# Optimization experiments

Hardware: AMD Instinct MI355X
Metric: run time of the kernel (lower is better)

Reference implementation:

```python
import jax, jax.numpy as jnp
import numpy as np

B, T, E, H, V = 64, 21, 512, 512, 10000


def _lstm_step(x, h, c, W_ih, W_hh, b):
    # PyTorch LSTMCell gate order: i, f, g, o
    gates = x @ W_ih.T + h @ W_hh.T + b  # [B, 4H]
    i, f, g, o = jnp.split(gates, 4, axis=-1)
    i, f, o = jax.nn.sigmoid(i), jax.nn.sigmoid(f), jax.nn.sigmoid(o)
    g = jnp.tanh(g)
    c_new = f * c + i * g
    h_new = o * jnp.tanh(c_new)
    return h_new, c_new


def setup_inputs() -> dict:
    key = jax.random.key(0)
    ks = jax.random.split(key, 8)
    s_ih = 1.0 / np.sqrt(H)
    return {
        "features": jax.random.normal(ks[0], (B, E), jnp.float32),
        "caption_embedding": jax.random.normal(ks[1], (B, T, E), jnp.float32),
        "W_ih": jax.random.uniform(ks[2], (4 * H, E), jnp.float32, -s_ih, s_ih),
        "W_hh": jax.random.uniform(ks[3], (4 * H, H), jnp.float32, -s_ih, s_ih),
        "b_ih": jax.random.uniform(ks[4], (4 * H,), jnp.float32, -s_ih, s_ih),
        "b_hh": jax.random.uniform(ks[5], (4 * H,), jnp.float32, -s_ih, s_ih),
        "W_lin": jax.random.uniform(ks[6], (V, H), jnp.float32, -s_ih, s_ih),
        "b_lin": jax.random.uniform(ks[7], (V,), jnp.float32, -s_ih, s_ih),
    }


def reference(features, caption_embedding, W_ih, W_hh, b_ih, b_hh, W_lin, b_lin):
    b = b_ih + b_hh
    batch = features.shape[0]
    hidden = W_hh.shape[1]
    h0 = jnp.zeros((batch, hidden), features.dtype)
    c0 = jnp.zeros((batch, hidden), features.dtype)
    # t = 0: consume image features, no output emitted
    h, c = _lstm_step(features, h0, c0, W_ih, W_hh, b)
    # t = 1..T-1: consume caption_embedding[:, t-1], emit linear(h)
    emb_seq = jnp.swapaxes(caption_embedding[:, :-1, :], 0, 1)  # [T-1, B, E]

    def body(carry, x_t):
        h, c = carry
        h, c = _lstm_step(x_t, h, c, W_ih, W_hh, b)
        out = h @ W_lin.T + b_lin  # [B, V]
        return (h, c), out

    _, outs = jax.lax.scan(body, (h, c), emb_seq)  # [T-1, B, V]
    return jnp.swapaxes(outs, 0, 1)  # [B, T-1, V]
```

## Files before the change

### kernel.cpp

```cpp
#include <hip/hip_runtime.h>
#include <hip/hip_bf16.h>


#define NB 64
#define NT 21
#define NE 512
#define NH 512
#define NV 10000
#define G4 2048
#define FLGD 16

typedef __attribute__((ext_vector_type(8))) short bf16x8;
typedef __attribute__((ext_vector_type(4))) float f32x4;
typedef __attribute__((ext_vector_type(4))) unsigned short u16x4;

#define OFF_WIH_HI   0UL
#define OFF_WIH_LO   2097152UL
#define OFF_WHH_HI   4194304UL
#define OFF_WHH_LO   6291456UL
#define OFF_WLIN_HI  8388608UL
#define OFF_XSEQ_HI  18743296UL
#define OFF_XSEQ_LO  20185088UL
#define OFF_BIAS     21626880UL
#define OFF_XIH      21635072UL
#define OFF_GHH      32645120UL
#define OFF_GHL      32776192UL
#define OFF_C        32907264UL
#define OFF_HBUF     33038336UL
#define OFF_FLG      34349056UL

__device__ inline unsigned short f2bf(float f) {
    unsigned int u = __float_as_uint(f);
    unsigned int r = u + 0x7FFFu + ((u >> 16) & 1u);
    return (unsigned short)(r >> 16);
}
__device__ inline float bf2f(unsigned short s) {
    return __uint_as_float(((unsigned int)s) << 16);
}

__device__ __forceinline__ void gl_lds16(const unsigned short* g, unsigned short* l) {
    auto gp = (const __attribute__((address_space(1))) unsigned int*)(unsigned long long)(const void*)g;
    auto lp = (__attribute__((address_space(3))) unsigned int*)(unsigned int)(unsigned long long)(void*)l;
    __builtin_amdgcn_global_load_lds(gp, lp, 16, 0, 0);
}

__device__ __forceinline__ void gl_lds16_sc(const unsigned short* g, unsigned short* l) {
    auto gp = (const __attribute__((address_space(1))) unsigned int*)(unsigned long long)(const void*)g;
    auto lp = (__attribute__((address_space(3))) unsigned int*)(unsigned int)(unsigned long long)(void*)l;
    __builtin_amdgcn_global_load_lds(gp, lp, 16, 0, 17);
}

__device__ __forceinline__ void st4_sc(unsigned int* p, unsigned int v) {
    asm volatile("global_store_dword %0, %1, off sc0 sc1" :: "v"(p), "v"(v) : "memory");
}
__device__ __forceinline__ void st8_sc(unsigned short* p, u16x4 v) {
    asm volatile("global_store_dwordx2 %0, %1, off sc0 sc1" :: "v"(p), "v"(v) : "memory");
}
__device__ __forceinline__ void st16_sc(float* p, f32x4 v) {
    asm volatile("global_store_dwordx4 %0, %1, off sc0 sc1" :: "v"(p), "v"(v) : "memory");
}

__global__ __launch_bounds__(512) void fused_all(
    const float* __restrict__ features, const float* __restrict__ cap,
    const float* __restrict__ W_ih_f, const float* __restrict__ W_hh_f,
    const float* __restrict__ b_ih, const float* __restrict__ b_hh,
    const float* __restrict__ W_lin_f, const float* __restrict__ b_lin,
    float* __restrict__ out, unsigned char* __restrict__ ws)
{
    __shared__ unsigned short Hhi[64 * 512];
    __shared__ unsigned short Hlo[64 * 512];
    __shared__ float glf[4096];
    const int tid = threadIdx.x;
    const int lane = tid & 63, wv = tid >> 6;
    const int mf = lane & 15, kg = lane >> 4;

    unsigned int* __restrict__ flg = (unsigned int*)(ws + OFF_C);
    unsigned int* __restrict__ slabctr = (unsigned int*)(ws + OFF_FLG);
    unsigned short* __restrict__ hbuf = (unsigned short*)(ws + OFF_HBUF);
    const float* __restrict__ bias = (const float*)(ws + OFF_BIAS);
    float* __restrict__ xih_base = (float*)(ws + OFF_XIH);

    {
        unsigned short* wih_hi = (unsigned short*)(ws + OFF_WIH_HI);
        unsigned short* wih_lo = (unsigned short*)(ws + OFF_WIH_LO);
        unsigned short* xs_hi = (unsigned short*)(ws + OFF_XSEQ_HI);
        unsigned short* xs_lo = (unsigned short*)(ws + OFF_XSEQ_LO);
        float* bias_w = (float*)(ws + OFF_BIAS);
        int idx = blockIdx.x * 512 + tid;
        for (int it = 0; it < 4; ++it, idx += 131072) {
            if (idx < 262144) {
                const int i4 = idx * 4;
                float4 w = *(const float4*)(W_ih_f + i4);
                u16x4 hi, lo;
                hi.x = f2bf(w.x); lo.x = f2bf(w.x - bf2f(hi.x));
                hi.y = f2bf(w.y); lo.y = f2bf(w.y - bf2f(hi.y));
                hi.z = f2bf(w.z); lo.z = f2bf(w.z - bf2f(hi.z));
                hi.w = f2bf(w.w); lo.w = f2bf(w.w - bf2f(hi.w));
                st8_sc(wih_hi + i4, hi);
                st8_sc(wih_lo + i4, lo);
            } else if (idx < 434176) {
                const int i4 = (idx - 262144) * 4;
                const int e = i4 & 511;
                const int b = (i4 >> 9) & 63;
                const int t2 = i4 >> 15;
                float4 x = (t2 == 0) ? *(const float4*)(features + b * NE + e)
                                     : *(const float4*)(cap + b * (NT * NE) + (t2 - 1) * NE + e);
                u16x4 hi, lo;
                hi.x = f2bf(x.x); lo.x = f2bf(x.x - bf2f(hi.x));
                hi.y = f2bf(x.y); lo.y = f2bf(x.y - bf2f(hi.y));
                hi.z = f2bf(x.z); lo.z = f2bf(x.z - bf2f(hi.z));
                hi.w = f2bf(x.w); lo.w = f2bf(x.w - bf2f(hi.w));
                st8_sc(xs_hi + i4, hi);
                st8_sc(xs_lo + i4, lo);
            } else if (idx < 434688) {
                const int j = (idx - 434176) * 4;
                float4 a = *(const float4*)(b_ih + j);
                float4 b = *(const float4*)(b_hh + j);
                f32x4 s;
                s[0] = a.x + b.x; s[1] = a.y + b.y; s[2] = a.z + b.z; s[3] = a.w + b.w;
                st16_sc(bias_w + j, s);
            }
        }
        asm volatile("s_waitcnt vmcnt(0)" ::: "memory");
        __syncthreads();
        if (tid == 0)
            __hip_atomic_fetch_add(&slabctr[24 * FLGD], 1u, __ATOMIC_RELAXED, __HIP_MEMORY_SCOPE_AGENT);
    }

    if (blockIdx.x < 32) {
        const int bc = blockIdx.x;
        const int q = wv & 3;
        const int mh = wv >> 2;

        unsigned short* __restrict__ ghh = (unsigned short*)(ws + OFF_GHH);
        unsigned short* __restrict__ ghl = (unsigned short*)(ws + OFF_GHL);

        bf16x8 bh[16], blo[16];
#pragma unroll
        for (int j = 0; j < 16; ++j) {
            const float* src = W_hh_f + (size_t)(q * 512 + bc * 16 + mf) * 512 + j * 32 + kg * 8;
            float4 w0 = *(const float4*)src;
            float4 w1 = *(const float4*)(src + 4);
            float ff[8] = {w0.x, w0.y, w0.z, w0.w, w1.x, w1.y, w1.z, w1.w};
#pragma unroll
            for (int e = 0; e < 8; ++e) {
                const unsigned short h = f2bf(ff[e]);
                bh[j][e] = (short)h;
                blo[j][e] = (short)f2bf(ff[e] - bf2f(h));
            }
        }

        const int crow = tid >> 3;
        const int cp = tid & 7;
        const int c0 = bc * 16 + cp * 2;
        const int jc0 = c0 >> 3;
        float creg0 = 0.f, creg1 = 0.f;

        float2 xp[4];
        auto load_xp = [&](int tt) {
            const float* __restrict__ xq = xih_base + (size_t)tt * NB * G4;
#pragma unroll
            for (int g2 = 0; g2 < 4; ++g2)
                xp[g2] = *(const float2*)&xq[crow * G4 + g2 * 512 + c0];
        };

        if (tid == 0) {
            while (__hip_atomic_load(&slabctr[0], __ATOMIC_RELAXED, __HIP_MEMORY_SCOPE_AGENT) < 16u)
                __builtin_amdgcn_s_sleep(1);
        }
        __syncthreads();
        load_xp(0);

        for (int t = 0; t < NT; ++t) {
            f32x4 acc[2];
            acc[0] = (f32x4){0.f, 0.f, 0.f, 0.f};
            acc[1] = (f32x4){0.f, 0.f, 0.f, 0.f};

            if (t > 0) {
                const int rd = (t + 1) & 1;
                const unsigned short* __restrict__ ghh_r = ghh + rd * (NB * NH);
                const unsigned short* __restrict__ ghl_r = ghl + rd * (NB * NH);
#pragma unroll
                for (int i = 0; i < 8; ++i) {
                    const int s = i * 512 + tid;
                    gl_lds16_sc(ghh_r + s * 8, &Hhi[s * 8]);
                }
#pragma unroll
                for (int i = 0; i < 8; ++i) {
                    const int s = i * 512 + tid;
                    gl_lds16_sc(ghl_r + s * 8, &Hlo[s * 8]);
                }
                asm volatile("s_waitcnt vmcnt(8)" ::: "memory");
                __builtin_amdgcn_s_barrier();
#pragma unroll
                for (int kt = 0; kt < 16; ++kt) {
                    const int j = kt * 4 + kg;
#pragma unroll
                    for (int m = 0; m < 2; ++m) {
                        const int row = mh * 32 + m * 16 + mf;
                        bf16x8 a_hi = *(const bf16x8*)&Hhi[(row * 64 + (j ^ (row & 7))) * 8];
                        acc[m] = __builtin_amdgcn_mfma_f32_16x16x32_bf16(a_hi, bh[kt], acc[m], 0, 0, 0);
                        acc[m] = __builtin_amdgcn_mfma_f32_16x16x32_bf16(a_hi, blo[kt], acc[m], 0, 0, 0);
                    }
                }
                asm volatile("s_waitcnt vmcnt(0)" ::: "memory");
                __builtin_amdgcn_s_barrier();
#pragma unroll
                for (int kt = 0; kt < 16; ++kt) {
                    const int j = kt * 4 + kg;
#pragma unroll
                    for (int m = 0; m < 2; ++m) {
                        const int row = mh * 32 + m * 16 + mf;
                        bf16x8 a_lo = *(const bf16x8*)&Hlo[(row * 64 + (j ^ (row & 7))) * 8];
                        acc[m] = __builtin_amdgcn_mfma_f32_16x16x32_bf16(a_lo, bh[kt], acc[m], 0, 0, 0);
                    }
                }
            }

#pragma unroll
            for (int m = 0; m < 2; ++m) {
                const int row = mh * 32 + m * 16 + kg * 4;
#pragma unroll
                for (int r = 0; r < 4; ++r)
                    glf[(q * 64 + row + r) * 16 + mf] = acc[m][r];
            }
            __syncthreads();

            {
                unsigned short* __restrict__ ghh_w = ghh + (t & 1) * (NB * NH);
                unsigned short* __restrict__ ghl_w = ghl + (t & 1) * (NB * NH);
                const float2 g0 = *(const float2*)&glf[(0 * 64 + crow) * 16 + cp * 2];
                const float2 g1 = *(const float2*)&glf[(1 * 64 + crow) * 16 + cp * 2];
                const float2 g2 = *(const float2*)&glf[(2 * 64 + crow) * 16 + cp * 2];
                const float2 g3 = *(const float2*)&glf[(3 * 64 + crow) * 16 + cp * 2];
                const float gi0 = g0.x + xp[0].x, gi1 = g0.y + xp[0].y;
                const float gf0 = g1.x + xp[1].x, gf1 = g1.y + xp[1].y;
                const float gg0 = g2.x + xp[2].x, gg1 = g2.y + xp[2].y;
                const float go0 = g3.x + xp[3].x, go1 = g3.y + xp[3].y;
                const float i0 = 1.f / (1.f + __expf(-gi0)), i1 = 1.f / (1.f + __expf(-gi1));
                const float f0 = 1.f / (1.f + __expf(-gf0)), f1 = 1.f / (1.f + __expf(-gf1));
                const float ga0 = tanhf(gg0),                ga1 = tanhf(gg1);
                const float o0 = 1.f / (1.f + __expf(-go0)), o1 = 1.f / (1.f + __expf(-go1));
                const float cn0 = f0 * creg0 + i0 * ga0;
                const float cn1 = f1 * creg1 + i1 * ga1;
                creg0 = cn0; creg1 = cn1;
                const float h0 = o0 * tanhf(cn0);
                const float h1 = o1 * tanhf(cn1);
                const unsigned short hi0 = f2bf(h0), hi1 = f2bf(h1);
                const unsigned short lo0 = f2bf(h0 - bf2f(hi0)), lo1 = f2bf(h1 - bf2f(hi1));
                const unsigned int hpack = (unsigned int)hi0 | ((unsigned int)hi1 << 16);
                const unsigned int lpack = (unsigned int)lo0 | ((unsigned int)lo1 << 16);
                const int sw = crow * 512 + ((jc0 ^ (crow & 7)) << 3) + (cp & 3) * 2;
                st4_sc((unsigned int*)&ghh_w[sw], hpack);
                st4_sc((unsigned int*)&ghl_w[sw], lpack);
                if (t >= 1)
                    st4_sc((unsigned int*)&hbuf[(size_t)(t - 1) * (NB * NH) + crow * NH + c0], hpack);
            }

            asm volatile("s_waitcnt vmcnt(0)" ::: "memory");
            __syncthreads();
            if (tid == 0) {
                unsigned int one = 1u;
                unsigned int* fp = flg + ((size_t)t * 32 + bc) * FLGD;
                asm volatile("global_store_dword %0, %1, off sc0 sc1" :: "v"(fp), "v"(one) : "memory");
            }
            if (t < NT - 1) {
                if (wv == 0) {
                    if (lane < 32) {
                        const unsigned int* fp = flg + ((size_t)t * 32 + lane) * FLGD;
                        while (__hip_atomic_load(fp, __ATOMIC_RELAXED, __HIP_MEMORY_SCOPE_AGENT) == 0u)
                            __builtin_amdgcn_s_sleep(1);
                    } else if (lane == 32) {
                        const unsigned int* sp = slabctr + (size_t)(t + 1) * FLGD;
                        while (__hip_atomic_load(sp, __ATOMIC_RELAXED, __HIP_MEMORY_SCOPE_AGENT) < 16u)
                            __builtin_amdgcn_s_sleep(1);
                    }
                }
                __syncthreads();
                load_xp(t + 1);
            }
        }
        asm volatile("s_waitcnt vmcnt(0)" ::: "memory");
        return;
    }

    const int g = blockIdx.x - 32;
    const int mw2 = (wv >> 2) * 32, nw2 = (wv & 3) * 32;

    if (tid == 0) {
        while (__hip_atomic_load(&slabctr[24 * FLGD], __ATOMIC_RELAXED, __HIP_MEMORY_SCOPE_AGENT) < 256u)
            __builtin_amdgcn_s_sleep(1);
    }
    __syncthreads();

    {
        const unsigned short* __restrict__ xh = (const unsigned short*)(ws + OFF_XSEQ_HI);
        const unsigned short* __restrict__ xl = (const unsigned short*)(ws + OFF_XSEQ_LO);
        const unsigned short* __restrict__ wih_h = (const unsigned short*)(ws + OFF_WIH_HI);
        const unsigned short* __restrict__ wih_l = (const unsigned short*)(ws + OFF_WIH_LO);

        unsigned short* Ah2 = Hhi;
        unsigned short* Al2 = Hhi + 4096;
        unsigned short* Bh2 = Hhi + 8192;
        unsigned short* Bl2 = Hhi + 16384;

        const int ntile = (g < 112) ? 2 : 1;
        for (int p = 0; p < ntile; ++p) {
            const int T = (p == 0) ? g : 224 + g;
            const int slab = T >> 4, ct = T & 15;
            const unsigned short* __restrict__ xhA = xh + (size_t)slab * 64 * 512;
            const unsigned short* __restrict__ xlA = xl + (size_t)slab * 64 * 512;

            auto stageA = [&](int buf, int k0) {
                if (tid < 256) {
                    const int s = tid, r = s >> 2, kc = (s & 3) * 8;
                    gl_lds16(xhA + (size_t)r * 512 + k0 + kc, &Ah2[buf * 2048 + s * 8]);
                    gl_lds16(xlA + (size_t)r * 512 + k0 + kc, &Al2[buf * 2048 + s * 8]);
                } else {
#pragma unroll
                    for (int h2 = 0; h2 < 2; ++h2) {
                        const int s = h2 * 256 + (tid - 256), r = s >> 2, kc = (s & 3) * 8;
                        gl_lds16(wih_h + (size_t)(ct * 128 + r) * 512 + k0 + kc, &Bh2[buf * 4096 + s * 8]);
                        gl_lds16(wih_l + (size_t)(ct * 128 + r) * 512 + k0 + kc, &Bl2[buf * 4096 + s * 8]);
                    }
                }
            };

            f32x4 acc2[2][2];
#pragma unroll
            for (int i = 0; i < 2; i++)
#pragma unroll
                for (int j = 0; j < 2; j++) acc2[i][j] = (f32x4){0.f, 0.f, 0.f, 0.f};

            stageA(0, 0);
            for (int kt = 0; kt < 16; ++kt) {
                __syncthreads();
                const int cur = kt & 1;
                if (kt < 15) stageA(cur ^ 1, (kt + 1) * 32);
                bf16x8 ah_[2], al_[2], bh_[2], bl_[2];
#pragma unroll
                for (int i = 0; i < 2; i++) {
                    ah_[i] = *(const bf16x8*)&Ah2[cur * 2048 + (mw2 + i * 16 + mf) * 32 + kg * 8];
                    al_[i] = *(const bf16x8*)&Al2[cur * 2048 + (mw2 + i * 16 + mf) * 32 + kg * 8];
                    bh_[i] = *(const bf16x8*)&Bh2[cur * 4096 + (nw2 + i * 16 + mf) * 32 + kg * 8];
                    bl_[i] = *(const bf16x8*)&Bl2[cur * 4096 + (nw2 + i * 16 + mf) * 32 + kg * 8];
                }
#pragma unroll
                for (int i = 0; i < 2; i++)
#pragma unroll
                    for (int j = 0; j < 2; j++) {
                        acc2[i][j] = __builtin_amdgcn_mfma_f32_16x16x32_bf16(ah_[i], bh_[j], acc2[i][j], 0, 0, 0);
                        acc2[i][j] = __builtin_amdgcn_mfma_f32_16x16x32_bf16(ah_[i], bl_[j], acc2[i][j], 0, 0, 0);
                        acc2[i][j] = __builtin_amdgcn_mfma_f32_16x16x32_bf16(al_[i], bh_[j], acc2[i][j], 0, 0, 0);
                    }
            }
#pragma unroll
            for (int i = 0; i < 2; i++)
#pragma unroll
                for (int j = 0; j < 2; j++) {
                    const int col = ct * 128 + nw2 + j * 16 + mf;
                    const float bb = bias[col];
#pragma unroll
                    for (int r = 0; r < 4; r++) {
                        const int row = slab * 64 + mw2 + i * 16 + kg * 4 + r;
                        st4_sc((unsigned int*)&xih_base[(size_t)row * G4 + col],
                               __float_as_uint(acc2[i][j][r] + bb));
                    }
                }
            asm volatile("s_waitcnt vmcnt(0)" ::: "memory");
            __syncthreads();
            if (tid == 0)
                __hip_atomic_fetch_add(&slabctr[slab * FLGD], 1u, __ATOMIC_RELAXED, __HIP_MEMORY_SCOPE_AGENT);
            __syncthreads();
        }
    }

    {
        unsigned short* wlin_w = (unsigned short*)(ws + OFF_WLIN_HI);
        int idx = g * 512 + tid;
        for (int it = 0; it < 12; ++it, idx += 114688) {
            if (idx < 1280000) {
                const int i4 = idx * 4;
                float4 w = *(const float4*)(W_lin_f + i4);
                u16x4 hi;
                hi.x = f2bf(w.x); hi.y = f2bf(w.y); hi.z = f2bf(w.z); hi.w = f2bf(w.w);
                st8_sc(wlin_w + i4, hi);
            }
        }
        asm volatile("s_waitcnt vmcnt(0)" ::: "memory");
        __syncthreads();
        if (tid == 0) {
            __hip_atomic_fetch_add(&slabctr[25 * FLGD], 1u, __ATOMIC_RELAXED, __HIP_MEMORY_SCOPE_AGENT);
            while (__hip_atomic_load(&slabctr[25 * FLGD], __ATOMIC_RELAXED, __HIP_MEMORY_SCOPE_AGENT) < 224u)
                __builtin_amdgcn_s_sleep(1);
        }
        __syncthreads();
    }

    const unsigned short* __restrict__ wlin = (const unsigned short*)(ws + OFF_WLIN_HI);
    const int jt = g % 79;
    const int rshare = g / 79;
    const int nshare = (jt < 66) ? 3 : 2;
    const int n0g = jt * 128;

    unsigned short* __restrict__ AsB = Hhi;
    unsigned short* __restrict__ BsB = Hhi + 4096;

    for (int tt = rshare; tt < NT - 1; tt += nshare) {
        if (wv == 0) {
            const unsigned int* fp = flg + ((size_t)(tt + 1) * 32 + (lane & 31)) * FLGD;
            while (__hip_atomic_load(fp, __ATOMIC_RELAXED, __HIP_MEMORY_SCOPE_AGENT) == 0u)
                __builtin_amdgcn_s_sleep(2);
        }
        __syncthreads();

        const unsigned short* __restrict__ hbA = hbuf + (size_t)tt * (NB * NH);
        auto stageC = [&](int buf, int k0) {
            if (tid < 256) {
                const int s = tid;
                const int r = s >> 2, kcol = (s & 3) * 8;
                gl_lds16_sc(hbA + (size_t)r * 512 + k0 + kcol, &AsB[buf * 2048 + s * 8]);
            } else {
#pragma unroll
                for (int h2 = 0; h2 < 2; ++h2) {
                    const int s = h2 * 256 + (tid - 256);
                    const int r = s >> 2, kcol = (s & 3) * 8;
                    gl_lds16(wlin + (size_t)(n0g + r) * 512 + k0 + kcol, &BsB[buf * 4096 + s * 8]);
                }
            }
        };

        f32x4 acc2[2][2];
#pragma unroll
        for (int i = 0; i < 2; i++)
#pragma unroll
            for (int j = 0; j < 2; j++) acc2[i][j] = (f32x4){0.f, 0.f, 0.f, 0.f};

        stageC(0, 0);
        for (int kt = 0; kt < 16; ++kt) {
            __syncthreads();
            const int cur = kt & 1;
            if (kt < 15) stageC(cur ^ 1, (kt + 1) * 32);
            bf16x8 af[2], bfv[2];
#pragma unroll
            for (int i = 0; i < 2; i++) {
                af[i]  = *(const bf16x8*)&AsB[cur * 2048 + (mw2 + i * 16 + mf) * 32 + kg * 8];
                bfv[i] = *(const bf16x8*)&BsB[cur * 4096 + (nw2 + i * 16 + mf) * 32 + kg * 8];
            }
#pragma unroll
            for (int i = 0; i < 2; i++)
#pragma unroll
                for (int j = 0; j < 2; j++)
                    acc2[i][j] = __builtin_amdgcn_mfma_f32_16x16x32_bf16(af[i], bfv[j], acc2[i][j], 0, 0, 0);
        }
#pragma unroll
        for (int i = 0; i < 2; i++)
#pragma unroll
            for (int j = 0; j < 2; j++) {
                const int col = n0g + nw2 + j * 16 + mf;
                if (col < NV) {
                    const float bl = b_lin[col];
#pragma unroll
                    for (int r = 0; r < 4; r++) {
                        const int b_ = mw2 + i * 16 + kg * 4 + r;
                        out[(size_t)b_ * ((NT - 1) * NV) + (size_t)tt * NV + col] = acc2[i][j][r] + bl;
                    }
                }
            }
        __syncthreads();
    }
}

extern "C" void kernel_launch(void* const* d_in, const int* in_sizes, int n_in,
                              void* d_out, int out_size, void* d_ws, size_t ws_size,
                              hipStream_t stream)
{
    const float* features = (const float*)d_in[0];
    const float* cap      = (const float*)d_in[1];
    const float* W_ih     = (const float*)d_in[2];
    const float* W_hh     = (const float*)d_in[3];
    const float* b_ih     = (const float*)d_in[4];
    const float* b_hh     = (const float*)d_in[5];
    const float* W_lin    = (const float*)d_in[6];
    const float* b_lin    = (const float*)d_in[7];
    float* out = (float*)d_out;
    unsigned char* ws = (unsigned char*)d_ws;

    (void)hipMemsetAsync(ws + OFF_C, 0, (size_t)NT * 32 * FLGD * sizeof(unsigned int), stream);
    (void)hipMemsetAsync(ws + OFF_FLG, 0, (size_t)32 * FLGD * sizeof(unsigned int), stream);

    hipLaunchKernelGGL(fused_all, dim3(256), dim3(512), 0, stream,
                       features, cap, W_ih, W_hh, b_ih, b_hh, W_lin, b_lin, out, ws);
}
```

Measured before the change: 269.1 us.

## Move recurrent blocks off weight-conversion prologue and split per-wave flag waits

The 32 recurrent LSTM blocks now skip the shared bf16 hi/lo conversion prologue and start immediately. Only the 224 GEMM blocks do the conversion, with a rebuilt stride and a barrier count of 224. Inside the recurrence, each wave now waits only on the 4 producer flags whose h chunks it loads, then copies those chunks to LDS itself. The h layout changes from a row-major swizzle to a chunk-major layout so each wave's slice is contiguous. This is meant to cut the prologue delay on the serial critical path and the single-wave all-flags barrier per step. The cost is a different LDS read pattern that may bring bank conflicts, and a moved x-projection load.

```diff
diff --git a/kernel.cpp b/kernel.cpp
--- a/kernel.cpp
+++ b/kernel.cpp
@@ -80,14 +80,172 @@
     const float* __restrict__ bias = (const float*)(ws + OFF_BIAS);
     float* __restrict__ xih_base = (float*)(ws + OFF_XIH);
 
+    if (blockIdx.x < 32) {
+        const int bc = blockIdx.x;
+        const int q = wv & 3;
+        const int mh = wv >> 2;
+
+        unsigned short* __restrict__ ghh = (unsigned short*)(ws + OFF_GHH);
+        unsigned short* __restrict__ ghl = (unsigned short*)(ws + OFF_GHL);
+
+        bf16x8 bh[16], blo[16];
+#pragma unroll
+        for (int j = 0; j < 16; ++j) {
+            const float* src = W_hh_f + (size_t)(q * 512 + bc * 16 + mf) * 512 + j * 32 + kg * 8;
+            float4 w0 = *(const float4*)src;
+            float4 w1 = *(const float4*)(src + 4);
+            float ff[8] = {w0.x, w0.y, w0.z, w0.w, w1.x, w1.y, w1.z, w1.w};
+#pragma unroll
+            for (int e = 0; e < 8; ++e) {
+                const unsigned short h = f2bf(ff[e]);
+                bh[j][e] = (short)h;
+                blo[j][e] = (short)f2bf(ff[e] - bf2f(h));
+            }
+        }
+
+        const int crow = tid >> 3;
+        const int cp = tid & 7;
+        const int c0 = bc * 16 + cp * 2;
+        const int jch = bc * 2 + (cp >> 2);
+        const int sw = (jch * 64 + crow) * 8 + ((cp * 2) & 7);
+        float creg0 = 0.f, creg1 = 0.f;
+
+        float2 xp[4];
+        auto load_xp = [&](int tt) {
+            const float* __restrict__ xq = xih_base + (size_t)tt * NB * G4;
+#pragma unroll
+            for (int g2 = 0; g2 < 4; ++g2)
+                xp[g2] = *(const float2*)&xq[crow * G4 + g2 * 512 + c0];
+        };
+
+        if (tid == 0) {
+            while (__hip_atomic_load(&slabctr[0], __ATOMIC_RELAXED, __HIP_MEMORY_SCOPE_AGENT) < 16u)
+                __builtin_amdgcn_s_sleep(1);
+        }
+        __syncthreads();
+        load_xp(0);
+
+        for (int t = 0; t < NT; ++t) {
+            f32x4 acc[2];
+            acc[0] = (f32x4){0.f, 0.f, 0.f, 0.f};
+            acc[1] = (f32x4){0.f, 0.f, 0.f, 0.f};
+
+            if (t > 0) {
+                const int rd = (t + 1) & 1;
+                const unsigned short* __restrict__ ghh_r = ghh + rd * (NB * NH);
+                const unsigned short* __restrict__ ghl_r = ghl + rd * (NB * NH);
+
+                if (lane < 4) {
+                    const unsigned int* fp = flg + ((size_t)(t - 1) * 32 + wv * 4 + lane) * FLGD;
+                    while (__hip_atomic_load(fp, __ATOMIC_RELAXED, __HIP_MEMORY_SCOPE_AGENT) == 0u)
+                        __builtin_amdgcn_s_sleep(1);
+                } else if (lane == 4) {
+                    const unsigned int* sp = slabctr + (size_t)t * FLGD;
+                    while (__hip_atomic_load(sp, __ATOMIC_RELAXED, __HIP_MEMORY_SCOPE_AGENT) < 16u)
+                        __builtin_amdgcn_s_sleep(1);
+                }
+#pragma unroll
+                for (int pp = 0; pp < 4; ++pp) {
+                    const int jj = (wv * 4 + pp) * 2;
+                    gl_lds16_sc(ghh_r + (jj    ) * 512 + lane * 8, &Hhi[(jj    ) * 512 + lane * 8]);
+                    gl_lds16_sc(ghh_r + (jj + 1) * 512 + lane * 8, &Hhi[(jj + 1) * 512 + lane * 8]);
+                }
+#pragma unroll
+                for (int pp = 0; pp < 4; ++pp) {
+                    const int jj = (wv * 4 + pp) * 2;
+                    gl_lds16_sc(ghl_r + (jj    ) * 512 + lane * 8, &Hlo[(jj    ) * 512 + lane * 8]);
+                    gl_lds16_sc(ghl_r + (jj + 1) * 512 + lane * 8, &Hlo[(jj + 1) * 512 + lane * 8]);
+                }
+                asm volatile("s_waitcnt vmcnt(8)" ::: "memory");
+                __builtin_amdgcn_s_barrier();
+                load_xp(t);
+#pragma unroll
+                for (int kt = 0; kt < 16; ++kt) {
+                    const int j = kt * 4 + kg;
+#pragma unroll
+                    for (int m = 0; m < 2; ++m) {
+                        const int row = mh * 32 + m * 16 + mf;
+                        bf16x8 a_hi = *(const bf16x8*)&Hhi[(j * 64 + row) * 8];
+                        acc[m] = __builtin_amdgcn_mfma_f32_16x16x32_bf16(a_hi, bh[kt], acc[m], 0, 0, 0);
+                        acc[m] = __builtin_amdgcn_mfma_f32_16x16x32_bf16(a_hi, blo[kt], acc[m], 0, 0, 0);
+                    }
+                }
+                asm volatile("s_waitcnt vmcnt(0)" ::: "memory");
+                __builtin_amdgcn_s_barrier();
+#pragma unroll
+                for (int kt = 0; kt < 16; ++kt) {
+                    const int j = kt * 4 + kg;
+#pragma unroll
+                    for (int m = 0; m < 2; ++m) {
+                        const int row = mh * 32 + m * 16 + mf;
+                        bf16x8 a_lo = *(const bf16x8*)&Hlo[(j * 64 + row) * 8];
+                        acc[m] = __builtin_amdgcn_mfma_f32_16x16x32_bf16(a_lo, bh[kt], acc[m], 0, 0, 0);
+                    }
+                }
+            }
+
+#pragma unroll
+            for (int m = 0; m < 2; ++m) {
+                const int row = mh * 32 + m * 16 + kg * 4;
+#pragma unroll
+                for (int r = 0; r < 4; ++r)
+                    glf[(q * 64 + row + r) * 16 + mf] = acc[m][r];
+            }
+            __syncthreads();
+
+            {
+                unsigned short* __restrict__ ghh_w = ghh + (t & 1) * (NB * NH);
+                unsigned short* __restrict__ ghl_w = ghl + (t & 1) * (NB * NH);
+                const float2 g0 = *(const float2*)&glf[(0 * 64 + crow) * 16 + cp * 2];
+                const float2 g1 = *(const float2*)&glf[(1 * 64 + crow) * 16 + cp * 2];
+                const float2 g2 = *(const float2*)&glf[(2 * 64 + crow) * 16 + cp * 2];
+                const float2 g3 = *(const float2*)&glf[(3 * 64 + crow) * 16 + cp * 2];
+                const float gi0 = g0.x + xp[0].x, gi1 = g0.y + xp[0].y;
+                const float gf0 = g1.x + xp[1].x, gf1 = g1.y + xp[1].y;
+                const float gg0 = g2.x + xp[2].x, gg1 = g2.y + xp[2].y;
+                const float go0 = g3.x + xp[3].x, go1 = g3.y + xp[3].y;
+                const float i0 = 1.f / (1.f + __expf(-gi0)), i1 = 1.f / (1.f + __expf(-gi1));
+                const float f0 = 1.f / (1.f + __expf(-gf0)), f1 = 1.f / (1.f + __expf(-gf1));
+                const float ga0 = tanhf(gg0),                ga1 = tanhf(gg1);
+                const float o0 = 1.f / (1.f + __expf(-go0)), o1 = 1.f / (1.f + __expf(-go1));
+                const float cn0 = f0 * creg0 + i0 * ga0;
+                const float cn1 = f1 * creg1 + i1 * ga1;
+                creg0 = cn0; creg1 = cn1;
+                const float h0 = o0 * tanhf(cn0);
+                const float h1 = o1 * tanhf(cn1);
+                const unsigned short hi0 = f2bf(h0), hi1 = f2bf(h1);
+                const unsigned short lo0 = f2bf(h0 - bf2f(hi0)), lo1 = f2bf(h1 - bf2f(hi1));
+                const unsigned int hpack = (unsigned int)hi0 | ((unsigned int)hi1 << 16);
+                const unsigned int lpack = (unsigned int)lo0 | ((unsigned int)lo1 << 16);
+                st4_sc((unsigned int*)&ghh_w[sw], hpack);
+                st4_sc((unsigned int*)&ghl_w[sw], lpack);
+                if (t >= 1)
+                    st4_sc((unsigned int*)&hbuf[(size_t)(t - 1) * (NB * NH) + crow * NH + c0], hpack);
+            }
+
+            asm volatile("s_waitcnt vmcnt(0)" ::: "memory");
+            __syncthreads();
+            if (tid == 0) {
+                unsigned int one = 1u;
+                unsigned int* fp = flg + ((size_t)t * 32 + bc) * FLGD;
+                asm volatile("global_store_dword %0, %1, off sc0 sc1" :: "v"(fp), "v"(one) : "memory");
+            }
+        }
+        asm volatile("s_waitcnt vmcnt(0)" ::: "memory");
+        return;
+    }
+
+    const int g = blockIdx.x - 32;
+    const int mw2 = (wv >> 2) * 32, nw2 = (wv & 3) * 32;
+
     {
         unsigned short* wih_hi = (unsigned short*)(ws + OFF_WIH_HI);
         unsigned short* wih_lo = (unsigned short*)(ws + OFF_WIH_LO);
         unsigned short* xs_hi = (unsigned short*)(ws + OFF_XSEQ_HI);
         unsigned short* xs_lo = (unsigned short*)(ws + OFF_XSEQ_LO);
         float* bias_w = (float*)(ws + OFF_BIAS);
-        int idx = blockIdx.x * 512 + tid;
-        for (int it = 0; it < 4; ++it, idx += 131072) {
+        int idx = g * 512 + tid;
+        for (int it = 0; it < 4; ++it, idx += 114688) {
             if (idx < 262144) {
                 const int i4 = idx * 4;
                 float4 w = *(const float4*)(W_ih_f + i4);
@@ -123,175 +281,13 @@
         }
         asm volatile("s_waitcnt vmcnt(0)" ::: "memory");
         __syncthreads();
-        if (tid == 0)
+        if (tid == 0) {
             __hip_atomic_fetch_add(&slabctr[24 * FLGD], 1u, __ATOMIC_RELAXED, __HIP_MEMORY_SCOPE_AGENT);
+            while (__hip_atomic_load(&slabctr[24 * FLGD], __ATOMIC_RELAXED, __HIP_MEMORY_SCOPE_AGENT) < 224u)
+                __builtin_amdgcn_s_sleep(1);
+        }
+        __syncthreads();
     }
-
-    if (blockIdx.x < 32) {
-        const int bc = blockIdx.x;
-        const int q = wv & 3;
-        const int mh = wv >> 2;
-
-        unsigned short* __restrict__ ghh = (unsigned short*)(ws + OFF_GHH);
-        unsigned short* __restrict__ ghl = (unsigned short*)(ws + OFF_GHL);
-
-        bf16x8 bh[16], blo[16];
-#pragma unroll
-        for (int j = 0; j < 16; ++j) {
-            const float* src = W_hh_f + (size_t)(q * 512 + bc * 16 + mf) * 512 + j * 32 + kg * 8;
-            float4 w0 = *(const float4*)src;
-            float4 w1 = *(const float4*)(src + 4);
-            float ff[8] = {w0.x, w0.y, w0.z, w0.w, w1.x, w1.y, w1.z, w1.w};
-#pragma unroll
-            for (int e = 0; e < 8; ++e) {
-                const unsigned short h = f2bf(ff[e]);
-                bh[j][e] = (short)h;
-                blo[j][e] = (short)f2bf(ff[e] - bf2f(h));
-            }
-        }
-
-        const int crow = tid >> 3;
-        const int cp = tid & 7;
-        const int c0 = bc * 16 + cp * 2;
-        const int jc0 = c0 >> 3;
-        float creg0 = 0.f, creg1 = 0.f;
-
-        float2 xp[4];
-        auto load_xp = [&](int tt) {
-            const float* __restrict__ xq = xih_base + (size_t)tt * NB * G4;
-#pragma unroll
-            for (int g2 = 0; g2 < 4; ++g2)
-                xp[g2] = *(const float2*)&xq[crow * G4 + g2 * 512 + c0];
-        };
-
-        if (tid == 0) {
-            while (__hip_atomic_load(&slabctr[0], __ATOMIC_RELAXED, __HIP_MEMORY_SCOPE_AGENT) < 16u)
-                __builtin_amdgcn_s_sleep(1);
-        }
-        __syncthreads();
-        load_xp(0);
-
-        for (int t = 0; t < NT; ++t) {
-            f32x4 acc[2];
-            acc[0] = (f32x4){0.f, 0.f, 0.f, 0.f};
-            acc[1] = (f32x4){0.f, 0.f, 0.f, 0.f};
-
-            if (t > 0) {
-                const int rd = (t + 1) & 1;
-                const unsigned short* __restrict__ ghh_r = ghh + rd * (NB * NH);
-                const unsigned short* __restrict__ ghl_r = ghl + rd * (NB * NH);
-#pragma unroll
-                for (int i = 0; i < 8; ++i) {
-                    const int s = i * 512 + tid;
-                    gl_lds16_sc(ghh_r + s * 8, &Hhi[s * 8]);
-                }
-#pragma unroll
-                for (int i = 0; i < 8; ++i) {
-                    const int s = i * 512 + tid;
-                    gl_lds16_sc(ghl_r + s * 8, &Hlo[s * 8]);
-                }
-                asm volatile("s_waitcnt vmcnt(8)" ::: "memory");
-                __builtin_amdgcn_s_barrier();
-#pragma unroll
-                for (int kt = 0; kt < 16; ++kt) {
-                    const int j = kt * 4 + kg;
-#pragma unroll
-                    for (int m = 0; m < 2; ++m) {
-                        const int row = mh * 32 + m * 16 + mf;
-                        bf16x8 a_hi = *(const bf16x8*)&Hhi[(row * 64 + (j ^ (row & 7))) * 8];
-                        acc[m] = __builtin_amdgcn_mfma_f32_16x16x32_bf16(a_hi, bh[kt], acc[m], 0, 0, 0);
-                        acc[m] = __builtin_amdgcn_mfma_f32_16x16x32_bf16(a_hi, blo[kt], acc[m], 0, 0, 0);
-                    }
-                }
-                asm volatile("s_waitcnt vmcnt(0)" ::: "memory");
-                __builtin_amdgcn_s_barrier();
-#pragma unroll
-                for (int kt = 0; kt < 16; ++kt) {
-                    const int j = kt * 4 + kg;
-#pragma unroll
-                    for (int m = 0; m < 2; ++m) {
-                        const int row = mh * 32 + m * 16 + mf;
-                        bf16x8 a_lo = *(const bf16x8*)&Hlo[(row * 64 + (j ^ (row & 7))) * 8];
-                        acc[m] = __builtin_amdgcn_mfma_f32_16x16x32_bf16(a_lo, bh[kt], acc[m], 0, 0, 0);
-                    }
-                }
-            }
-
-#pragma unroll
-            for (int m = 0; m < 2; ++m) {
-                const int row = mh * 32 + m * 16 + kg * 4;
-#pragma unroll
-                for (int r = 0; r < 4; ++r)
-                    glf[(q * 64 + row + r) * 16 + mf] = acc[m][r];
-            }
-            __syncthreads();
-
-            {
-                unsigned short* __restrict__ ghh_w = ghh + (t & 1) * (NB * NH);
-                unsigned short* __restrict__ ghl_w = ghl + (t & 1) * (NB * NH);
-                const float2 g0 = *(const float2*)&glf[(0 * 64 + crow) * 16 + cp * 2];
-                const float2 g1 = *(const float2*)&glf[(1 * 64 + crow) * 16 + cp * 2];
-                const float2 g2 = *(const float2*)&glf[(2 * 64 + crow) * 16 + cp * 2];
-                const float2 g3 = *(const float2*)&glf[(3 * 64 + crow) * 16 + cp * 2];
-                const float gi0 = g0.x + xp[0].x, gi1 = g0.y + xp[0].y;
-                const float gf0 = g1.x + xp[1].x, gf1 = g1.y + xp[1].y;
-                const float gg0 = g2.x + xp[2].x, gg1 = g2.y + xp[2].y;
-                const float go0 = g3.x + xp[3].x, go1 = g3.y + xp[3].y;
-                const float i0 = 1.f / (1.f + __expf(-gi0)), i1 = 1.f / (1.f + __expf(-gi1));
-                const float f0 = 1.f / (1.f + __expf(-gf0)), f1 = 1.f / (1.f + __expf(-gf1));
-                const float ga0 = tanhf(gg0),                ga1 = tanhf(gg1);
-                const float o0 = 1.f / (1.f + __expf(-go0)), o1 = 1.f / (1.f + __expf(-go1));
-                const float cn0 = f0 * creg0 + i0 * ga0;
-                const float cn1 = f1 * creg1 + i1 * ga1;
-                creg0 = cn0; creg1 = cn1;
-                const float h0 = o0 * tanhf(cn0);
-                const float h1 = o1 * tanhf(cn1);
-                const unsigned short hi0 = f2bf(h0), hi1 = f2bf(h1);
-                const unsigned short lo0 = f2bf(h0 - bf2f(hi0)), lo1 = f2bf(h1 - bf2f(hi1));
-                const unsigned int hpack = (unsigned int)hi0 | ((unsigned int)hi1 << 16);
-                const unsigned int lpack = (unsigned int)lo0 | ((unsigned int)lo1 << 16);
-                const int sw = crow * 512 + ((jc0 ^ (crow & 7)) << 3) + (cp & 3) * 2;
-                st4_sc((unsigned int*)&ghh_w[sw], hpack);
-                st4_sc((unsigned int*)&ghl_w[sw], lpack);
-                if (t >= 1)
-                    st4_sc((unsigned int*)&hbuf[(size_t)(t - 1) * (NB * NH) + crow * NH + c0], hpack);
-            }
-
-            asm volatile("s_waitcnt vmcnt(0)" ::: "memory");
-            __syncthreads();
-            if (tid == 0) {
-                unsigned int one = 1u;
-                unsigned int* fp = flg + ((size_t)t * 32 + bc) * FLGD;
-                asm volatile("global_store_dword %0, %1, off sc0 sc1" :: "v"(fp), "v"(one) : "memory");
-            }
-            if (t < NT - 1) {
-                if (wv == 0) {
-                    if (lane < 32) {
-                        const unsigned int* fp = flg + ((size_t)t * 32 + lane) * FLGD;
-                        while (__hip_atomic_load(fp, __ATOMIC_RELAXED, __HIP_MEMORY_SCOPE_AGENT) == 0u)
-                            __builtin_amdgcn_s_sleep(1);
-                    } else if (lane == 32) {
-                        const unsigned int* sp = slabctr + (size_t)(t + 1) * FLGD;
-                        while (__hip_atomic_load(sp, __ATOMIC_RELAXED, __HIP_MEMORY_SCOPE_AGENT) < 16u)
-                            __builtin_amdgcn_s_sleep(1);
-                    }
-                }
-                __syncthreads();
-                load_xp(t + 1);
-            }
-        }
-        asm volatile("s_waitcnt vmcnt(0)" ::: "memory");
-        return;
-    }
-
-    const int g = blockIdx.x - 32;
-    const int mw2 = (wv >> 2) * 32, nw2 = (wv & 3) * 32;
-
-    if (tid == 0) {
-        while (__hip_atomic_load(&slabctr[24 * FLGD], __ATOMIC_RELAXED, __HIP_MEMORY_SCOPE_AGENT) < 256u)
-            __builtin_amdgcn_s_sleep(1);
-    }
-    __syncthreads();
 
     {
         const unsigned short* __restrict__ xh = (const unsigned short*)(ws + OFF_XSEQ_HI);
```

Measured after the change: 262.6 us. -2.4%, faster.
